# Optimization experiments

Hardware: AMD Instinct MI355X
Metric: run time of the kernel (lower is better)

The kernel has to match this reference:

```python
import jax, jax.numpy as jnp
import numpy as np

LN_EPS = 1e-12


def _layernorm(x, g, b):
    mu = jnp.mean(x, axis=-1, keepdims=True)
    var = jnp.mean(jnp.square(x - mu), axis=-1, keepdims=True)
    return (x - mu) * jax.lax.rsqrt(var + LN_EPS) * g + b


def setup_inputs() -> dict:
    key = jax.random.key(0)
    ks = jax.random.split(key, 8)
    A, EP, H, HI, D = 64, 8, 768, 1536, 100
    Etot = A * EP
    return {
        "E": jax.random.normal(ks[0], (A, Etot, H), dtype=jnp.float32),
        "W1": jax.random.normal(ks[1], (H, HI), dtype=jnp.float32) * 0.02,
        "b1": jnp.zeros((HI,), jnp.float32),
        "ln_g": jnp.ones((HI,), jnp.float32),
        "ln_b": jnp.zeros((HI,), jnp.float32),
        "W2": jax.random.normal(ks[2], (HI, D), dtype=jnp.float32) * 0.02,
        "b2": jnp.zeros((D,), jnp.float32),
        "entity_count": 8,  # uniform entities per step (static)
    }


def reference(E, W1, b1, ln_g, ln_b, W2, b2, entity_count):
    A, Etot, H = E.shape
    EP = int(entity_count)
    D = W2.shape[1]

    # VG head: Linear -> exact GELU -> LayerNorm(eps=1e-12) -> Linear
    h = E.reshape(-1, H) @ W1 + b1                       # [A*Etot, 2H]
    h = _layernorm(jax.nn.gelu(h, approximate=False), ln_g, ln_b)
    logits = h @ W2 + b2                                 # [A*Etot, D]
    # reshape(A, Etot, D).permute(1,0,2) -> [Etot, A, D]
    VG_logits = logits.reshape(A, Etot, D).transpose(1, 0, 2)

    # per-entity logits at its own step: idx_2 = step index of each entity
    steps_of = jnp.arange(Etot) // EP                    # [Etot]
    own = VG_logits[jnp.arange(Etot), steps_of]          # [Etot, D]
    VG_scores = jnp.max(jax.nn.softmax(own, axis=-1), axis=-1)  # [Etot]
    VG_scores_index = jnp.argmax(own, axis=-1)           # [Etot] (argmax of softmax == argmax of logits)

    # Faithful to original loop: b stays -1 (`bbox = b+1` never updates b),
    # so every valid score gathers detection VG_scores_index[-1].
    sel = VG_scores_index[-1]
    # entity e=(m,j) -> VG_logits[e, l, sel]; uniform counts => all (j,k) valid
    g = VG_logits[:, :, sel].reshape(A, EP, A)           # [m, j, l]
    scores = jnp.broadcast_to(
        g.transpose(2, 0, 1)[:, :, :, None], (A, A, EP, EP)
    )                                                    # [l, m, j, k]
    scores = scores[None]                                # [1, A, A, EP, EP]

    VG_scores_index_padded = VG_scores_index.reshape(A, EP)
    return scores, VG_scores, VG_scores_index_padded
```

## Files before the change

kernel.cpp:

```cpp
#include <hip/hip_runtime.h>
#include <hip/hip_bf16.h>
#include <math.h>


typedef __bf16 bf16_t;
typedef __bf16  bf16x8  __attribute__((ext_vector_type(8)));
typedef float   floatx4 __attribute__((ext_vector_type(4)));

__device__ __forceinline__ float gelu_exact(float x) {
    return 0.5f * x * (1.0f + erff(x * 0.7071067811865475f));
}
__device__ __forceinline__ float gelu_fast(float x) {
    const float z = x * (1.0f + 0.044715f * x * x);
    return __fdividef(x, 1.0f + __expf(-1.5957691216f * z));
}

__device__ __forceinline__ void gl_lds16(const void* g, void* l) {
    __builtin_amdgcn_global_load_lds(
        (const __attribute__((address_space(1))) void*)g,
        (__attribute__((address_space(3))) void*)l, 16, 0, 0);
}

__global__ __launch_bounds__(256) void prep_duo(
        const float* __restrict__ E, const float* __restrict__ W1,
        bf16_t* __restrict__ W1t, float* __restrict__ hpart,
        bf16_t* __restrict__ Ebf) {
    __shared__ alignas(16) char smemc[16640];
    const int bid = blockIdx.x;
    const int tid = threadIdx.x;

    if (bid >= 1056) {
        const int cb = bid - 1056;
        const size_t base = ((size_t)cb * 256 + tid) * 8;
        const float4 v0 = *(const float4*)(E + base);
        const float4 v1 = *(const float4*)(E + base + 4);
        bf16x8 o;
        o[0] = (bf16_t)v0.x; o[1] = (bf16_t)v0.y;
        o[2] = (bf16_t)v0.z; o[3] = (bf16_t)v0.w;
        o[4] = (bf16_t)v1.x; o[5] = (bf16_t)v1.y;
        o[6] = (bf16_t)v1.z; o[7] = (bf16_t)v1.w;
        *(bf16x8*)(Ebf + base) = o;
        return;
    }

    if (bid < 288) {
        float* sT = (float*)smemc;
        const int bk = bid % 12, bn = bid / 12;
        const int k0 = bk * 64, n0 = bn * 64;
        #pragma unroll
        for (int i = 0; i < 16; ++i) {
            const int idx = tid + i * 256;
            const int kk = idx >> 6, nn = idx & 63;
            sT[kk * 65 + nn] = W1[(size_t)(k0 + kk) * 1536 + n0 + nn];
        }
        __syncthreads();
        #pragma unroll
        for (int i = 0; i < 16; ++i) {
            const int idx = tid + i * 256;
            const int nn = idx >> 6, kk = idx & 63;
            W1t[(size_t)(n0 + nn) * 768 + k0 + kk] = (bf16_t)sT[kk * 65 + nn];
        }
    } else {
        float* sE = (float*)smemc;
        const int b  = bid - 288;
        const int a  = b & 63;
        const int rest = b >> 6;
        const int by = rest % 3, kq = rest / 3;

        const float* Ebase = E + (size_t)(520 * a) * 768 + kq * 192;
        for (int idx = tid; idx < 1536; idx += 256) {
            const int row = idx / 192, i = idx - row * 192;
            sE[idx] = Ebase[(size_t)row * 768 + i];
        }
        __syncthreads();

        const int c0 = by * 512 + tid * 2;
        const float* w1p = W1 + (size_t)(kq * 192) * 1536 + c0;
        float ax[8] = {}, ay[8] = {};
        for (int k = 0; k < 192; ++k) {
            const float2 w = *(const float2*)(w1p + (size_t)k * 1536);
            #pragma unroll
            for (int j = 0; j < 8; ++j) {
                const float e = sE[j * 192 + k];
                ax[j] += w.x * e;
                ay[j] += w.y * e;
            }
        }
        #pragma unroll
        for (int j = 0; j < 8; ++j)
            *(float2*)(hpart + (size_t)(kq * 512 + a * 8 + j) * 1536 + c0)
                = make_float2(ax[j], ay[j]);
    }
}

__global__ __launch_bounds__(256) void own_lnlog(
        const float* __restrict__ hpart, const float* __restrict__ b1,
        const float* __restrict__ lng,  const float* __restrict__ lnb,
        const float* __restrict__ W2,   const float* __restrict__ b2,
        float* __restrict__ own) {
    __shared__ float srow[1536];
    __shared__ float red8[8];
    __shared__ float redl[128];
    const int row = blockIdx.x, tid = threadIdx.x;
    const int lane = tid & 63, wv = tid >> 6;

    float x[6];
    #pragma unroll
    for (int i = 0; i < 6; ++i) {
        const int c = tid + i * 256;
        x[i] = gelu_exact(hpart[(size_t)row * 1536 + c]
                        + hpart[(size_t)(512 + row) * 1536 + c]
                        + hpart[(size_t)(1024 + row) * 1536 + c]
                        + hpart[(size_t)(1536 + row) * 1536 + c] + b1[c]);
    }
    float s = 0.f;
    #pragma unroll
    for (int i = 0; i < 6; ++i) s += x[i];
    #pragma unroll
    for (int o = 32; o > 0; o >>= 1) s += __shfl_xor(s, o, 64);
    if (lane == 0) red8[wv] = s;
    __syncthreads();
    const float mu = (red8[0] + red8[1] + red8[2] + red8[3]) * (1.0f / 1536.0f);

    float s2 = 0.f;
    #pragma unroll
    for (int i = 0; i < 6; ++i) { float d = x[i] - mu; s2 += d * d; }
    #pragma unroll
    for (int o = 32; o > 0; o >>= 1) s2 += __shfl_xor(s2, o, 64);
    if (lane == 0) red8[4 + wv] = s2;
    __syncthreads();
    const float rstd = rsqrtf((red8[4] + red8[5] + red8[6] + red8[7]) * (1.0f / 1536.0f) + 1e-12f);

    #pragma unroll
    for (int i = 0; i < 6; ++i) {
        const int c = tid + i * 256;
        srow[c] = (x[i] - mu) * rstd * lng[c] + lnb[c];
    }
    __syncthreads();

    const int d  = tid & 127;
    const int ks = tid >> 7;
    const int dd = d < 100 ? d : 99;
    float acc = ks ? 0.0f : b2[dd];
    const float* hr = srow + ks * 768;
    for (int k = 0; k < 768; ++k)
        acc += hr[k] * W2[(size_t)(ks * 768 + k) * 100 + dd];
    if (ks) redl[d] = acc;
    __syncthreads();
    if (!ks && d < 100) own[(size_t)row * 100 + d] = acc + redl[d];
}

__global__ __launch_bounds__(512) void finalize(
        const float* __restrict__ own, const float* __restrict__ W2,
        const float* __restrict__ b2,  const float* __restrict__ lng,
        const float* __restrict__ lnb, float* __restrict__ out,
        float* __restrict__ u, float* __restrict__ gwbw) {
    __shared__ int ssel;
    __shared__ float rg[8], rb[8];
    const int e = threadIdx.x;
    const int lane = e & 63, wv = e >> 6;
    const float* r = own + (size_t)e * 100;
    float best = r[0]; int bi = 0;
    for (int i = 1; i < 100; ++i) {
        const float v = r[i];
        if (v > best) { best = v; bi = i; }
    }
    float s = 0.f;
    for (int i = 0; i < 100; ++i) s += expf(r[i] - best);
    out[262144 + e] = 1.0f / s;
    out[262656 + e] = (float)bi;
    if (e == 511) ssel = bi;
    __syncthreads();
    const int sel = ssel;

    float gw = 0.f, bw = 0.f;
    #pragma unroll
    for (int c = e; c < 1536; c += 512) {
        const float wv2 = W2[(size_t)c * 100 + sel];
        const float uu = lng[c] * wv2;
        u[c] = uu;
        gw += uu;
        bw += lnb[c] * wv2;
    }
    #pragma unroll
    for (int o = 32; o > 0; o >>= 1) {
        gw += __shfl_xor(gw, o, 64);
        bw += __shfl_xor(bw, o, 64);
    }
    if (lane == 0) { rg[wv] = gw; rb[wv] = bw; }
    __syncthreads();
    if (e == 0) {
        float G = 0.f, B = 0.f;
        #pragma unroll
        for (int i = 0; i < 8; ++i) { G += rg[i]; B += rb[i]; }
        gwbw[0] = G;
        gwbw[1] = B + b2[sel];
    }
}

__global__ __launch_bounds__(256) void gemm1p(
        const bf16_t* __restrict__ A, const bf16_t* __restrict__ Bt,
        const float* __restrict__ bias, const float* __restrict__ u,
        float* __restrict__ pS1, float* __restrict__ pS2,
        float* __restrict__ pD) {
    constexpr int K = 768;
    __shared__ alignas(16) char smem[36864];
    bf16_t* sA = (bf16_t*)smem;
    bf16_t* sB = (bf16_t*)(smem + 16384);

    const int linear = blockIdx.x + gridDim.x * blockIdx.y;
    const int xcd  = linear & 7;
    const int slot = linear >> 3;
    const int bx = slot % gridDim.x;
    const int by = (slot / gridDim.x) * 8 + xcd;

    const int tid  = threadIdx.x;
    const int lane = tid & 63;
    const int wave = tid >> 6;
    const int wr = wave >> 1, wc = wave & 1;
    const int m0 = by * 128;
    const int n0 = bx * 128;
    const int q  = lane >> 4;
    const int l15 = lane & 15;

    const bf16_t* gA[4]; bf16_t* lA[4];
    const bf16_t* gB[4]; bf16_t* lB[4];
    #pragma unroll
    for (int c = 0; c < 4; ++c) {
        const int s    = c * 256 + tid;
        const int row  = s >> 3;
        const int col  = s & 7;
        const int gcol = col ^ (row & 7);
        gA[c] = A  + (size_t)(m0 + row) * K + gcol * 8;
        lA[c] = sA + (c * 256 + wave * 64) * 8;
        gB[c] = Bt + (size_t)(n0 + row) * K + gcol * 8;
        lB[c] = sB + (c * 256 + wave * 64) * 8;
    }
    const bf16_t* rA[4]; const bf16_t* rB[4];
    #pragma unroll
    for (int t4 = 0; t4 < 4; ++t4) {
        rA[t4] = sA + (wr * 64 + t4 * 16 + l15) * 64;
        rB[t4] = sB + (wc * 64 + t4 * 16 + l15) * 64;
    }
    const int c0 = ((q)     ^ (lane & 7)) * 8;
    const int c1 = ((4 + q) ^ (lane & 7)) * 8;

    floatx4 acc[4][4] = {};

    #pragma unroll
    for (int kt = 0; kt < 12; ++kt) {
        const int k0 = kt * 64;
        __syncthreads();
        #pragma unroll
        for (int c = 0; c < 4; ++c) gl_lds16(gB[c] + k0, lB[c]);
        #pragma unroll
        for (int c = 0; c < 4; ++c) gl_lds16(gA[c] + k0, lA[c]);
        __syncthreads();

        #pragma unroll
        for (int ks = 0; ks < 2; ++ks) {
            const int co = ks ? c1 : c0;
            bf16x8 af[4], bfr[4];
            #pragma unroll
            for (int t4 = 0; t4 < 4; ++t4) {
                af[t4]  = *(const bf16x8*)(rA[t4] + co);
                bfr[t4] = *(const bf16x8*)(rB[t4] + co);
            }
            #pragma unroll
            for (int mt = 0; mt < 4; ++mt)
                #pragma unroll
                for (int nt = 0; nt < 4; ++nt)
                    acc[mt][nt] = __builtin_amdgcn_mfma_f32_16x16x32_bf16(
                        af[mt], bfr[nt], acc[mt][nt], 0, 0, 0);
        }
    }

    __syncthreads();
    bf16_t* sh = (bf16_t*)smem;
    float*  su = (float*)(smem + 33280);
    float*  sp = (float*)(smem + 33792);

    if (tid < 128) su[tid] = u[n0 + tid];
    float bias4[4];
    #pragma unroll
    for (int nt = 0; nt < 4; ++nt) bias4[nt] = bias[n0 + wc * 64 + nt * 16 + l15];

    #pragma unroll
    for (int mt = 0; mt < 4; ++mt)
        #pragma unroll
        for (int nt = 0; nt < 4; ++nt)
            #pragma unroll
            for (int r = 0; r < 4; ++r) {
                const int rowl = wr * 64 + mt * 16 + q * 4 + r;
                const int coll = wc * 64 + nt * 16 + l15;
                sh[rowl * 130 + coll] = (bf16_t)gelu_fast(acc[mt][nt][r] + bias4[nt]);
            }
    __syncthreads();

    {
        const int rowl = tid >> 1, half = tid & 1;
        const bf16_t* hp = sh + rowl * 130 + half * 64;
        const float*  up = su + half * 64;
        float s1 = 0.f, s2 = 0.f, dd = 0.f;
        #pragma unroll
        for (int c = 0; c < 64; ++c) {
            const float v = (float)hp[c];
            s1 += v; s2 += v * v; dd += v * up[c];
        }
        sp[tid * 3 + 0] = s1; sp[tid * 3 + 1] = s2; sp[tid * 3 + 2] = dd;
    }
    __syncthreads();
    if (tid < 128) {
        const float* p0 = sp + (2 * tid) * 3;
        const float* p1 = sp + (2 * tid + 1) * 3;
        const size_t idx = (size_t)bx * 32768 + (m0 + tid);
        pS1[idx] = p0[0] + p1[0];
        pS2[idx] = p0[1] + p1[1];
        pD[idx]  = p0[2] + p1[2];
    }
}

__global__ __launch_bounds__(256) void out_scores(
        const float* __restrict__ pS1, const float* __restrict__ pS2,
        const float* __restrict__ pD,  const float* __restrict__ gwbw,
        float* __restrict__ out) {
    const int t = blockIdx.x * 256 + threadIdx.x;
    float s1 = 0.f, s2 = 0.f, d = 0.f;
    #pragma unroll
    for (int nt = 0; nt < 12; ++nt) {
        const size_t idx = (size_t)nt * 32768 + t;
        s1 += pS1[idx]; s2 += pS2[idx]; d += pD[idx];
    }
    const float mu   = s1 * (1.0f / 1536.0f);
    const float var  = s2 * (1.0f / 1536.0f) - mu * mu;
    const float rstd = rsqrtf(var + 1e-12f);
    const float v = rstd * (d - mu * gwbw[0]) + gwbw[1];
    const float4 f = make_float4(v, v, v, v);
    float4* o = (float4*)(out + (size_t)t * 8);
    o[0] = f; o[1] = f;
}

extern "C" void kernel_launch(void* const* d_in, const int* in_sizes, int n_in,
                              void* d_out, int out_size, void* d_ws, size_t ws_size,
                              hipStream_t stream) {
    const float* E   = (const float*)d_in[0];
    const float* W1  = (const float*)d_in[1];
    const float* b1  = (const float*)d_in[2];
    const float* lng = (const float*)d_in[3];
    const float* lnb = (const float*)d_in[4];
    const float* W2  = (const float*)d_in[5];
    const float* b2  = (const float*)d_in[6];
    float* out = (float*)d_out;

    char* w = (char*)d_ws;
    auto carve = [&](size_t bytes) {
        void* p = (void*)w;
        w += (bytes + 255) & ~(size_t)255;
        return p;
    };
    bf16_t* W1t   = (bf16_t*)carve((size_t)1536 * 768 * 2);
    bf16_t* Ebf   = (bf16_t*)carve((size_t)32768 * 768 * 2);
    float*  own   = (float*)carve((size_t)512 * 100 * 4);
    float*  u     = (float*)carve(1536 * 4);
    float*  gwbw  = (float*)carve(256);
    char*   unionr = (char*)carve((size_t)4 * 512 * 1536 * 4);
    float*  hpart = (float*)unionr;
    float*  pS1   = (float*)unionr;
    float*  pS2   = (float*)(unionr + (size_t)12 * 32768 * 4);
    float*  pD    = (float*)(unionr + (size_t)24 * 32768 * 4);

    prep_duo<<<13344, 256, 0, stream>>>(E, W1, W1t, hpart, Ebf);
    own_lnlog<<<512, 256, 0, stream>>>(hpart, b1, lng, lnb, W2, b2, own);
    finalize<<<1, 512, 0, stream>>>(own, W2, b2, lng, lnb, out, u, gwbw);
    gemm1p<<<dim3(12, 256), 256, 0, stream>>>(Ebf, W1t, b1, u, pS1, pS2, pD);
    out_scores<<<128, 256, 0, stream>>>(pS1, pS2, pD, gwbw, out);
}
```

Before: 337.1 us.

## Fuse finalize into own_lnlog, widen block to 512, pack W1t stores

The single-block finalize kernel is folded into own_lnlog. Each row block now computes its own softmax max and argmax with wave shuffles, and the last row block (511) computes the u/gw/bw terms, which removes one launch and the serial 512-thread pass over the own buffer. own_lnlog now runs 512 threads that split the W2 dot product four ways. The W1 transpose stores bf16 pairs. This depends on row 511 being the entity whose argmax selects sel, which the reference also uses.

Measured after the change: 305.7 us. 1.1x faster.

```diff
diff --git a/kernel.cpp b/kernel.cpp
--- a/kernel.cpp
+++ b/kernel.cpp
@@ -4,6 +4,7 @@
 
 
 typedef __bf16 bf16_t;
+typedef __bf16  bf16x2  __attribute__((ext_vector_type(2)));
 typedef __bf16  bf16x8  __attribute__((ext_vector_type(8)));
 typedef float   floatx4 __attribute__((ext_vector_type(4)));
 
@@ -55,10 +56,14 @@
         }
         __syncthreads();
         #pragma unroll
-        for (int i = 0; i < 16; ++i) {
+        for (int i = 0; i < 8; ++i) {
             const int idx = tid + i * 256;
-            const int nn = idx >> 6, kk = idx & 63;
-            W1t[(size_t)(n0 + nn) * 768 + k0 + kk] = (bf16_t)sT[kk * 65 + nn];
+            const int nn = idx >> 5;
+            const int kp = (idx & 31) * 2;
+            bf16x2 v;
+            v[0] = (bf16_t)sT[kp * 65 + nn];
+            v[1] = (bf16_t)sT[(kp + 1) * 65 + nn];
+            *(bf16x2*)(W1t + (size_t)(n0 + nn) * 768 + k0 + kp) = v;
         }
     } else {
         float* sE = (float*)smemc;
@@ -93,47 +98,54 @@
     }
 }
 
-__global__ __launch_bounds__(256) void own_lnlog(
+__global__ __launch_bounds__(512) void own_lnlog(
         const float* __restrict__ hpart, const float* __restrict__ b1,
         const float* __restrict__ lng,  const float* __restrict__ lnb,
         const float* __restrict__ W2,   const float* __restrict__ b2,
-        float* __restrict__ own) {
+        float* __restrict__ out, float* __restrict__ u,
+        float* __restrict__ gwbw) {
     __shared__ float srow[1536];
-    __shared__ float red8[8];
-    __shared__ float redl[128];
+    __shared__ float red16[16];
+    __shared__ float redl[384];
+    __shared__ float slog[128];
+    __shared__ int   ssel;
     const int row = blockIdx.x, tid = threadIdx.x;
     const int lane = tid & 63, wv = tid >> 6;
 
-    float x[6];
-    #pragma unroll
-    for (int i = 0; i < 6; ++i) {
-        const int c = tid + i * 256;
+    float x[3];
+    #pragma unroll
+    for (int i = 0; i < 3; ++i) {
+        const int c = tid + i * 512;
         x[i] = gelu_exact(hpart[(size_t)row * 1536 + c]
                         + hpart[(size_t)(512 + row) * 1536 + c]
                         + hpart[(size_t)(1024 + row) * 1536 + c]
                         + hpart[(size_t)(1536 + row) * 1536 + c] + b1[c]);
     }
-    float s = 0.f;
-    #pragma unroll
-    for (int i = 0; i < 6; ++i) s += x[i];
+    float s = x[0] + x[1] + x[2];
     #pragma unroll
     for (int o = 32; o > 0; o >>= 1) s += __shfl_xor(s, o, 64);
-    if (lane == 0) red8[wv] = s;
-    __syncthreads();
-    const float mu = (red8[0] + red8[1] + red8[2] + red8[3]) * (1.0f / 1536.0f);
+    if (lane == 0) red16[wv] = s;
+    __syncthreads();
+    float mu = 0.f;
+    #pragma unroll
+    for (int i = 0; i < 8; ++i) mu += red16[i];
+    mu *= (1.0f / 1536.0f);
 
     float s2 = 0.f;
     #pragma unroll
-    for (int i = 0; i < 6; ++i) { float d = x[i] - mu; s2 += d * d; }
+    for (int i = 0; i < 3; ++i) { float d = x[i] - mu; s2 += d * d; }
     #pragma unroll
     for (int o = 32; o > 0; o >>= 1) s2 += __shfl_xor(s2, o, 64);
-    if (lane == 0) red8[4 + wv] = s2;
-    __syncthreads();
-    const float rstd = rsqrtf((red8[4] + red8[5] + red8[6] + red8[7]) * (1.0f / 1536.0f) + 1e-12f);
-
-    #pragma unroll
-    for (int i = 0; i < 6; ++i) {
-        const int c = tid + i * 256;
+    if (lane == 0) red16[8 + wv] = s2;
+    __syncthreads();
+    float v2 = 0.f;
+    #pragma unroll
+    for (int i = 0; i < 8; ++i) v2 += red16[8 + i];
+    const float rstd = rsqrtf(v2 * (1.0f / 1536.0f) + 1e-12f);
+
+    #pragma unroll
+    for (int i = 0; i < 3; ++i) {
+        const int c = tid + i * 512;
         srow[c] = (x[i] - mu) * rstd * lng[c] + lnb[c];
     }
     __syncthreads();
@@ -141,60 +153,66 @@
     const int d  = tid & 127;
     const int ks = tid >> 7;
     const int dd = d < 100 ? d : 99;
-    float acc = ks ? 0.0f : b2[dd];
-    const float* hr = srow + ks * 768;
-    for (int k = 0; k < 768; ++k)
-        acc += hr[k] * W2[(size_t)(ks * 768 + k) * 100 + dd];
-    if (ks) redl[d] = acc;
-    __syncthreads();
-    if (!ks && d < 100) own[(size_t)row * 100 + d] = acc + redl[d];
-}
-
-__global__ __launch_bounds__(512) void finalize(
-        const float* __restrict__ own, const float* __restrict__ W2,
-        const float* __restrict__ b2,  const float* __restrict__ lng,
-        const float* __restrict__ lnb, float* __restrict__ out,
-        float* __restrict__ u, float* __restrict__ gwbw) {
-    __shared__ int ssel;
-    __shared__ float rg[8], rb[8];
-    const int e = threadIdx.x;
-    const int lane = e & 63, wv = e >> 6;
-    const float* r = own + (size_t)e * 100;
-    float best = r[0]; int bi = 0;
-    for (int i = 1; i < 100; ++i) {
-        const float v = r[i];
-        if (v > best) { best = v; bi = i; }
-    }
-    float s = 0.f;
-    for (int i = 0; i < 100; ++i) s += expf(r[i] - best);
-    out[262144 + e] = 1.0f / s;
-    out[262656 + e] = (float)bi;
-    if (e == 511) ssel = bi;
-    __syncthreads();
-    const int sel = ssel;
-
-    float gw = 0.f, bw = 0.f;
-    #pragma unroll
-    for (int c = e; c < 1536; c += 512) {
-        const float wv2 = W2[(size_t)c * 100 + sel];
-        const float uu = lng[c] * wv2;
-        u[c] = uu;
-        gw += uu;
-        bw += lnb[c] * wv2;
-    }
-    #pragma unroll
-    for (int o = 32; o > 0; o >>= 1) {
-        gw += __shfl_xor(gw, o, 64);
-        bw += __shfl_xor(bw, o, 64);
-    }
-    if (lane == 0) { rg[wv] = gw; rb[wv] = bw; }
-    __syncthreads();
-    if (e == 0) {
-        float G = 0.f, B = 0.f;
-        #pragma unroll
-        for (int i = 0; i < 8; ++i) { G += rg[i]; B += rb[i]; }
-        gwbw[0] = G;
-        gwbw[1] = B + b2[sel];
+    float acc = (ks == 0) ? b2[dd] : 0.0f;
+    const float* hr  = srow + ks * 384;
+    const float* w2p = W2 + (size_t)(ks * 384) * 100 + dd;
+    #pragma unroll 8
+    for (int k = 0; k < 384; ++k)
+        acc += hr[k] * w2p[(size_t)k * 100];
+    if (ks) redl[(ks - 1) * 128 + d] = acc;
+    __syncthreads();
+    if (ks == 0) {
+        const float tot = acc + redl[d] + redl[128 + d] + redl[256 + d];
+        slog[d] = (d < 100) ? tot : -INFINITY;
+    }
+    __syncthreads();
+
+    if (wv == 0) {
+        const float v0 = slog[lane], v1 = slog[lane + 64];
+        float bv; int bi;
+        if (v0 >= v1) { bv = v0; bi = lane; } else { bv = v1; bi = lane + 64; }
+        #pragma unroll
+        for (int o = 1; o < 64; o <<= 1) {
+            const float vo = __shfl_xor(bv, o, 64);
+            const int   io = __shfl_xor(bi, o, 64);
+            if (vo > bv || (vo == bv && io < bi)) { bv = vo; bi = io; }
+        }
+        float e = expf(v0 - bv) + expf(v1 - bv);
+        #pragma unroll
+        for (int o = 32; o > 0; o >>= 1) e += __shfl_xor(e, o, 64);
+        if (lane == 0) {
+            out[262144 + row] = 1.0f / e;
+            out[262656 + row] = (float)bi;
+            ssel = bi;
+        }
+    }
+    __syncthreads();
+
+    if (row == 511) {
+        const int sel = ssel;
+        float gw = 0.f, bw = 0.f;
+        #pragma unroll
+        for (int c = tid; c < 1536; c += 512) {
+            const float wv2 = W2[(size_t)c * 100 + sel];
+            const float uu = lng[c] * wv2;
+            u[c] = uu;
+            gw += uu;
+            bw += lnb[c] * wv2;
+        }
+        #pragma unroll
+        for (int o = 32; o > 0; o >>= 1) {
+            gw += __shfl_xor(gw, o, 64);
+            bw += __shfl_xor(bw, o, 64);
+        }
+        if (lane == 0) { red16[wv] = gw; red16[8 + wv] = bw; }
+        __syncthreads();
+        if (tid == 0) {
+            float G = 0.f, B = 0.f;
+            #pragma unroll
+            for (int i = 0; i < 8; ++i) { G += red16[i]; B += red16[8 + i]; }
+            gwbw[0] = G;
+            gwbw[1] = B + b2[sel];
+        }
     }
 }
 
@@ -360,7 +378,6 @@
     };
     bf16_t* W1t   = (bf16_t*)carve((size_t)1536 * 768 * 2);
     bf16_t* Ebf   = (bf16_t*)carve((size_t)32768 * 768 * 2);
-    float*  own   = (float*)carve((size_t)512 * 100 * 4);
     float*  u     = (float*)carve(1536 * 4);
     float*  gwbw  = (float*)carve(256);
     char*   unionr = (char*)carve((size_t)4 * 512 * 1536 * 4);
@@ -370,8 +387,8 @@
     float*  pD    = (float*)(unionr + (size_t)24 * 32768 * 4);
 
     prep_duo<<<13344, 256, 0, stream>>>(E, W1, W1t, hpart, Ebf);
-    own_lnlog<<<512, 256, 0, stream>>>(hpart, b1, lng, lnb, W2, b2, own);
-    finalize<<<1, 512, 0, stream>>>(own, W2, b2, lng, lnb, out, u, gwbw);
+    own_lnlog<<<512, 512, 0, stream>>>(hpart, b1, lng, lnb, W2, b2,
+                                       out, u, gwbw);
     gemm1p<<<dim3(12, 256), 256, 0, stream>>>(Ebf, W1t, b1, u, pS1, pS2, pD);
     out_scores<<<128, 256, 0, stream>>>(pS1, pS2, pD, gwbw, out);
 }
```
